# Performance work log

Measured on AMD Instinct MI355X. Metric: run time of the kernel, lower is better.

## Reference

```python
import jax, jax.numpy as jnp
import numpy as np
import math

B, S, D = 2, 4096, 1024
H, HD = 16, 64
R = 16

def _rope(x, cos, sin):
    # x: [B, S, H, HD]; cos/sin: [S, HD//2]
    xr = x.reshape(*x.shape[:-1], HD // 2, 2)
    xe, xo = xr[..., 0], xr[..., 1]
    c = cos[None, :, None, :]
    s = sin[None, :, None, :]
    # complex multiply (xe + i*xo) * (c + i*s)
    re = xe * c - xo * s
    im = xe * s + xo * c
    return jnp.stack([re, im], axis=-1).reshape(x.shape)

def setup_inputs() -> dict:
    key = jax.random.key(0)
    ks = jax.random.split(key, 20)
    inp = {}
    inp["x"] = jax.random.normal(ks[0], (B, S, D), dtype=jnp.float32)
    pos = jnp.arange(S, dtype=jnp.float32)
    inv_freq = 1.0 / (10000.0 ** (jnp.arange(0, HD, 2, dtype=jnp.float32) / HD))
    ang = pos[:, None] * inv_freq[None, :]  # [S, HD//2]
    inp["freqs_cos"] = jnp.cos(ang)
    inp["freqs_sin"] = jnp.sin(ang)
    causal = jnp.triu(jnp.full((S, S), -1e9, dtype=jnp.float32), k=1)
    inp["mask"] = causal[None, None, :, :]
    sc = 1.0 / math.sqrt(D)
    inp["wq_w"] = jax.random.normal(ks[1], (D, D), dtype=jnp.float32) * sc
    inp["wq_b"] = jnp.zeros((D,), dtype=jnp.float32)
    inp["wk_w"] = jax.random.normal(ks[2], (D, D), dtype=jnp.float32) * sc
    inp["wv_w"] = jax.random.normal(ks[3], (D, D), dtype=jnp.float32) * sc
    inp["wo_w"] = jax.random.normal(ks[4], (D, D), dtype=jnp.float32) * sc
    inp["wo_b"] = jnp.zeros((D,), dtype=jnp.float32)
    for i, nm in enumerate(["q", "k", "v", "o"]):
        inp[f"lora_{nm}_l1"] = jax.random.normal(ks[5 + 2 * i], (R, D), dtype=jnp.float32) * sc
        inp[f"lora_{nm}_l2"] = jax.random.normal(ks[6 + 2 * i], (D, R), dtype=jnp.float32) * 0.01
    return inp

def reference(x, freqs_cos, freqs_sin, mask, wq_w, wq_b, wk_w, wv_w, wo_w, wo_b,
              lora_q_l1, lora_q_l2, lora_k_l1, lora_k_l2,
              lora_v_l1, lora_v_l2, lora_o_l1, lora_o_l2):
    # QKV projections + LoRA deltas (torch Linear: y = x @ W.T + b, W is [out, in])
    xq = x @ wq_w.T + wq_b + (x @ lora_q_l1.T) @ lora_q_l2.T
    xk = x @ wk_w.T + (x @ lora_k_l1.T) @ lora_k_l2.T
    xv = x @ wv_w.T + (x @ lora_v_l1.T) @ lora_v_l2.T
    xq = xq.reshape(B, S, H, HD)
    xk = xk.reshape(B, S, H, HD)
    xv = xv.reshape(B, S, H, HD)
    xq = _rope(xq, freqs_cos, freqs_sin)
    xk = _rope(xk, freqs_cos, freqs_sin)
    # attention (training path: keys/values = current xk/xv, causal mask additive)
    scores = jnp.einsum('bqhd,bkhd->bhqk', xq, xk) / math.sqrt(HD)
    scores = scores + mask
    probs = jax.nn.softmax(scores.astype(jnp.float32), axis=-1).astype(xq.dtype)
    out = jnp.einsum('bhqk,bkhd->bqhd', probs, xv).reshape(B, S, D)
    return out @ wo_w.T + wo_b + (out @ lora_o_l1.T) @ lora_o_l2.T
```

## Files before the change

kernel.cpp:

```cpp
#include <hip/hip_runtime.h>
#include <hip/hip_bf16.h>
#include <stdint.h>

#define S_DIM 4096
#define D_DIM 1024
#define KAUG  1088
#define M_ROWS 8192

typedef short bf16x8 __attribute__((ext_vector_type(8)));
typedef float f32x4  __attribute__((ext_vector_type(4)));

__device__ __forceinline__ f32x4 mfma16(bf16x8 a, bf16x8 b, f32x4 c) {
  return __builtin_amdgcn_mfma_f32_16x16x32_bf16(a, b, c, 0, 0, 0);
}
__device__ __forceinline__ short f2bs(float f) {
  __hip_bfloat16 h = __float2bfloat16(f);
  return *reinterpret_cast<short*>(&h);
}
__device__ __forceinline__ short f2bs_fast(float f) {
  unsigned u = __builtin_bit_cast(unsigned, f) + 0x8000u;
  return (short)(u >> 16);
}
__device__ __forceinline__ unsigned pk2bf(float a, float b) {
  unsigned ua = __builtin_bit_cast(unsigned, a) + 0x8000u;
  unsigned ub = __builtin_bit_cast(unsigned, b) + 0x8000u;
  return __builtin_amdgcn_perm(ub, ua, 0x07060302);
}
__device__ __forceinline__ float bs2f(short s) {
  __hip_bfloat16 h;
  *reinterpret_cast<short*>(&h) = s;
  return __bfloat162float(h);
}
__device__ __forceinline__ float fexp2(float x) {
  return __builtin_amdgcn_exp2f(x);
}
__device__ __forceinline__ void gload16(const void* g, void* l) {
  __builtin_amdgcn_global_load_lds(
      (const __attribute__((address_space(1))) unsigned int*)g,
      (__attribute__((address_space(3))) unsigned int*)l, 16, 0, 0);
}

__global__ void prep_k(const float* __restrict__ x,
                       const float* __restrict__ wq, const float* __restrict__ wk,
                       const float* __restrict__ wv, const float* __restrict__ wo,
                       const float* __restrict__ wqb,
                       const float* __restrict__ lq1, const float* __restrict__ lq2,
                       const float* __restrict__ lk1, const float* __restrict__ lk2,
                       const float* __restrict__ lv1, const float* __restrict__ lv2,
                       const float* __restrict__ lo1, const float* __restrict__ lo2,
                       const float* __restrict__ cf, const float* __restrict__ sf,
                       short* __restrict__ xaug, short* __restrict__ wqkv,
                       short* __restrict__ woaug, short* __restrict__ l1cat,
                       float* __restrict__ biasc, float* __restrict__ cs2)
{
  unsigned i = blockIdx.x * 256u + threadIdx.x;
  if (i < 8388608u) {
    unsigned m = i >> 10, k = i & 1023u;
    xaug[(size_t)m * KAUG + k] = f2bs(x[i]);
    return;
  }
  i -= 8388608u;
  if (i < 3342336u) {
    unsigned n = i / 1088u, k = i - n * 1088u;
    float v;
    if (k < 1024u) {
      v = (n < 1024u) ? wq[n * 1024u + k]
        : (n < 2048u) ? wk[(n - 1024u) * 1024u + k]
                      : wv[(n - 2048u) * 1024u + k];
    } else {
      unsigned r = k - 1024u, blk = r >> 4, which = n >> 10;
      if (blk == which) {
        const float* l2 = which == 0 ? lq2 : which == 1 ? lk2 : lv2;
        v = l2[(n & 1023u) * 16u + (r & 15u)];
      } else v = 0.f;
    }
    wqkv[i] = f2bs(v);
    return;
  }
  i -= 3342336u;
  if (i < 1114112u) {
    unsigned n = i / 1088u, k = i - n * 1088u;
    float v = (k < 1024u) ? wo[n * 1024u + k]
            : (k < 1040u) ? lo2[n * 16u + (k - 1024u)] : 0.f;
    woaug[i] = f2bs(v);
    return;
  }
  i -= 1114112u;
  if (i < 65536u) {
    unsigned r = i >> 10, k = i & 1023u;
    const float* src = r < 16u ? lq1 : r < 32u ? lk1 : r < 48u ? lv1 : lo1;
    l1cat[i] = f2bs(src[(r & 15u) * 1024u + k]);
    return;
  }
  i -= 65536u;
  if (i < 3072u) {
    biasc[i] = (i < 1024u) ? wqb[i] : 0.f;
    return;
  }
  i -= 3072u;
  if (i < 131072u) {
    cs2[2u * i]     = cf[i];
    cs2[2u * i + 1] = sf[i];
  }
}

template<int MODE>
__global__ __launch_bounds__(256) void gemm_bt(
    const short* __restrict__ A, int lda,
    const short* __restrict__ B, int ldb,
    int N, int K,
    const float* __restrict__ bias,
    void* __restrict__ Cout, int ldc, int colofs,
    short* __restrict__ qo, short* __restrict__ ko, short* __restrict__ vo,
    const float* __restrict__ cs2)
{
  __shared__ short As[2][128 * 32];
  __shared__ short Bs[2][128 * 32];
  const int tid = threadIdx.x;
  const int w = tid >> 6, lane = tid & 63;
  const int q4 = lane >> 4, c = lane & 15;
  const int mh = w >> 1, nh = w & 1;

  const int id = (int)blockIdx.y * gridDim.x + (int)blockIdx.x;
  const int g = id & 7, j = id >> 3;
  const int mt = g * 8 + (j & 7);
  const int nt = j >> 3;

  const int rl = lane >> 2;
  const int kc = (lane & 3) * 8;

  const short* Ag0 = A + (size_t)(mt * 128 + w * 32 + rl) * lda + kc;
  const short* Ag1 = Ag0 + (size_t)16 * lda;
  int rb0 = nt * 128 + w * 32 + rl;      if (rb0 > N - 1) rb0 = N - 1;
  int rb1 = nt * 128 + w * 32 + 16 + rl; if (rb1 > N - 1) rb1 = N - 1;
  const short* Bg0 = B + (size_t)rb0 * ldb + kc;
  const short* Bg1 = B + (size_t)rb1 * ldb + kc;
  const int sD0 = (w * 32) * 32;
  const int sD1 = (w * 32 + 16) * 32;

  f32x4 acc[4][4];
#pragma unroll
  for (int ms = 0; ms < 4; ++ms)
#pragma unroll
    for (int ns = 0; ns < 4; ++ns) acc[ms][ns] = (f32x4){0.f, 0.f, 0.f, 0.f};

  gload16(Ag0, &As[0][sD0]);
  gload16(Ag1, &As[0][sD1]);
  gload16(Bg0, &Bs[0][sD0]);
  gload16(Bg1, &Bs[0][sD1]);
  Ag0 += 32; Ag1 += 32; Bg0 += 32; Bg1 += 32;
  __syncthreads();

  const int nkt = K >> 5;
  for (int kt = 0; kt < nkt; ++kt) {
    const int cur = kt & 1, nxt = cur ^ 1;
    if (kt + 1 < nkt) {
      gload16(Ag0, &As[nxt][sD0]);
      gload16(Ag1, &As[nxt][sD1]);
      gload16(Bg0, &Bs[nxt][sD0]);
      gload16(Bg1, &Bs[nxt][sD1]);
      Ag0 += 32; Ag1 += 32; Bg0 += 32; Bg1 += 32;
    }
    bf16x8 af[4], bfr[4];
#pragma unroll
    for (int ms = 0; ms < 4; ++ms)
      af[ms] = *(const bf16x8*)&As[cur][(mh * 64 + ms * 16 + c) * 32 + q4 * 8];
#pragma unroll
    for (int ns = 0; ns < 4; ++ns)
      bfr[ns] = *(const bf16x8*)&Bs[cur][(nh * 64 + ns * 16 + c) * 32 + q4 * 8];
#pragma unroll
    for (int ms = 0; ms < 4; ++ms)
#pragma unroll
      for (int ns = 0; ns < 4; ++ns)
        acc[ms][ns] = mfma16(af[ms], bfr[ns], acc[ms][ns]);
    __syncthreads();
  }

#pragma unroll
  for (int ms = 0; ms < 4; ++ms) {
#pragma unroll
    for (int ns = 0; ns < 4; ++ns) {
      const int n = nt * 128 + nh * 64 + ns * 16 + c;
      if (MODE == 0) {
        float bsv = (n < N) ? bias[n] : 0.f;
        float* Co = (float*)Cout;
#pragma unroll
        for (int r = 0; r < 4; ++r) {
          int m = mt * 128 + mh * 64 + ms * 16 + q4 * 4 + r;
          if (n < N) Co[(size_t)m * ldc + n] = acc[ms][ns][r] + bsv;
        }
      } else if (MODE == 1) {
        short* Co = (short*)Cout;
#pragma unroll
        for (int r = 0; r < 4; ++r) {
          int m = mt * 128 + mh * 64 + ms * 16 + q4 * 4 + r;
          if (n < N) Co[(size_t)m * ldc + colofs + n] = f2bs_fast(acc[ms][ns][r]);
        }
      } else {
        float bsv = bias[n];
        int which = n >> 10;
        int m0 = mt * 128 + mh * 64 + ms * 16 + q4 * 4;
        int bb = m0 >> 12, spos = m0 & 4095;
        if (which < 2) {
          int h = (n >> 6) & 15;
          int hd = n & 63;
          short* dst = which == 0 ? qo : ko;
          const float sgn = (c & 1) ? 1.f : -1.f;
          const int ihalf = hd >> 1;
#pragma unroll
          for (int r = 0; r < 4; ++r) {
            float val = acc[ms][ns][r] + bsv;
            float part = __shfl_xor(val, 1);
            float2 cs = *(const float2*)&cs2[((size_t)(spos + r) * 32 + ihalf) * 2];
            float res = val * cs.x + part * (sgn * cs.y);
            if (which == 0) res *= 0.18033688011112042f;
            dst[(size_t)((bb * 16 + h) * 4096 + spos + r) * 64 + hd] = f2bs_fast(res);
          }
        } else {
          int h = (n >> 6) & 15;
          int hd = n & 63;
          uint2 vk;
          vk.x = pk2bf(acc[ms][ns][0] + bsv, acc[ms][ns][1] + bsv);
          vk.y = pk2bf(acc[ms][ns][2] + bsv, acc[ms][ns][3] + bsv);
          *(uint2*)&vo[(((size_t)bb * 16 + h) * 64 + hd) * 4096 + spos] = vk;
        }
      }
    }
  }
}

template<int NT>
__global__ __launch_bounds__(256) void tgemm_k(
    const short* __restrict__ A, int lda,
    const short* __restrict__ B, int ldb,
    int N, int K, short* __restrict__ C, int ldc, int colofs)
{
  __shared__ short As[2][64 * 32];
  __shared__ short Bs[2][64 * 32];
  const int tid = threadIdx.x;
  const int w = tid >> 6, lane = tid & 63;
  const int q4 = lane >> 4, c = lane & 15;
  const int rl = lane >> 2, kc = (lane & 3) * 8;
  const int arow = w * 16 + rl;
  const int brow = arow <= N - 1 ? arow : N - 1;

  const short* Ag = A + (size_t)(blockIdx.x * 64 + arow) * lda + kc;
  const short* Bg = B + (size_t)brow * ldb + kc;
  const int sD = (w * 16) * 32;

  f32x4 acc[NT];
#pragma unroll
  for (int i = 0; i < NT; ++i) acc[i] = (f32x4){0.f, 0.f, 0.f, 0.f};

  gload16(Ag, &As[0][sD]);
  gload16(Bg, &Bs[0][sD]);
  Ag += 32; Bg += 32;
  __syncthreads();

  const int nkt = K >> 5;
  for (int kt = 0; kt < nkt; ++kt) {
    const int cur = kt & 1, nxt = cur ^ 1;
    if (kt + 1 < nkt) {
      gload16(Ag, &As[nxt][sD]);
      gload16(Bg, &Bs[nxt][sD]);
      Ag += 32; Bg += 32;
    }
    bf16x8 af = *(const bf16x8*)&As[cur][(w * 16 + c) * 32 + q4 * 8];
#pragma unroll
    for (int nsi = 0; nsi < NT; ++nsi) {
      bf16x8 bf = *(const bf16x8*)&Bs[cur][(nsi * 16 + c) * 32 + q4 * 8];
      acc[nsi] = mfma16(af, bf, acc[nsi]);
    }
    __syncthreads();
  }
#pragma unroll
  for (int nsi = 0; nsi < NT; ++nsi) {
#pragma unroll
    for (int r = 0; r < 4; ++r) {
      int m = blockIdx.x * 64 + w * 16 + q4 * 4 + r;
      int n = nsi * 16 + c;
      if (n < N) C[(size_t)m * ldc + colofs + n] = f2bs_fast(acc[nsi][r]);
    }
  }
}

__global__ __launch_bounds__(256, 2) void flash_k(
    const short* __restrict__ Qb, const short* __restrict__ Kb,
    const short* __restrict__ Vt, short* __restrict__ Oaug)
{
  __shared__ short lds[24576];
  short* const PL = &lds[16384];

  const int id = (int)blockIdx.y * 16 + (int)blockIdx.x;
  const int g = id & 7, j = id >> 3;
  const int bh = g * 4 + (j >> 4);
  const int bx = j & 15;

  const int tid = threadIdx.x;
  const int w = tid >> 6, lane = tid & 63;
  const int q4 = lane >> 4, c = lane & 15;

  const short* Kg = Kb + (size_t)bh * 4096 * 64;
  const short* Vg = Vt + (size_t)bh * 64 * 4096;

  const int l8 = lane >> 3, l7 = lane & 7;
  const int sw = (l7 ^ l8) * 8;
  const int G0 = w * 2, G1 = w * 2 + 1;
  const int koff0 = (G0 * 8 + l8) * 64 + sw;
  const int koff1 = (G1 * 8 + l8) * 64 + sw;
  const int voff0 = (G0 * 8 + l8) * 4096 + sw;
  const int voff1 = (G1 * 8 + l8) * 4096 + sw;
  const int qg = w * 4;
  const int qoff0 = ((qg + 0) * 8 + l8) * 64 + sw;
  const int qoff1 = ((qg + 1) * 8 + l8) * 64 + sw;
  const int qoff2 = ((qg + 2) * 8 + l8) * 64 + sw;
  const int qoff3 = ((qg + 3) * 8 + l8) * 64 + sw;

  const int c7 = c & 7;
  const int chA0 = ((q4) ^ c7) * 8;
  const int chA1 = ((4 + q4) ^ c7) * 8;
  const int rowc = c * 64;
  const int rowq = (w * 16 + c) * 64;
  const int pw_base = (w * 16 + c) * 64 + (q4 & 1) * 4;
  const int pw_g = q4 >> 1;

  const int b = bh >> 4, h = bh & 15;

  for (int half = 0; half < 2; ++half) {
    const int qt = half == 0 ? 31 - bx : bx;
    const short* Qg = Qb + ((size_t)bh * 4096 + qt * 128) * 64;

    gload16(Qg + qoff0, &lds[16384 + (qg + 0) * 512]);
    gload16(Qg + qoff1, &lds[16384 + (qg + 1) * 512]);
    gload16(Qg + qoff2, &lds[16384 + (qg + 2) * 512]);
    gload16(Qg + qoff3, &lds[16384 + (qg + 3) * 512]);
    gload16(Kg + koff0, &lds[G0 * 512]);
    gload16(Kg + koff1, &lds[G1 * 512]);
    gload16(Vg + voff0, &lds[8192 + G0 * 512]);
    gload16(Vg + voff1, &lds[8192 + G1 * 512]);
    __syncthreads();

    bf16x8 qa0 = *(const bf16x8*)(PL + rowq + chA0);
    bf16x8 qa1 = *(const bf16x8*)(PL + rowq + chA1);
    bf16x8 qb0 = *(const bf16x8*)(PL + 4096 + rowq + chA0);
    bf16x8 qb1 = *(const bf16x8*)(PL + 4096 + rowq + chA1);

    f32x4 oa[4], ob[4];
#pragma unroll
    for (int i = 0; i < 4; ++i) {
      oa[i] = (f32x4){0.f, 0.f, 0.f, 0.f};
      ob[i] = (f32x4){0.f, 0.f, 0.f, 0.f};
    }
    float la = 0.f, lb = 0.f;

    const int last = 2 * qt + 1;
    for (int kt = 0; kt <= last; ++kt) {
      const int cur = (kt & 1) * 4096;
      const short* Kc = &lds[cur];
      const short* Vc = &lds[8192 + cur];
      if (kt < last) {
        const int nxt = ((kt + 1) & 1) * 4096;
        const short* ks = Kg + (size_t)(kt + 1) * 4096;
        const short* vs = Vg + (size_t)(kt + 1) * 64;
        gload16(ks + koff0, &lds[nxt + G0 * 512]);
        gload16(ks + koff1, &lds[nxt + G1 * 512]);
        gload16(vs + voff0, &lds[8192 + nxt + G0 * 512]);
        gload16(vs + voff1, &lds[8192 + nxt + G1 * 512]);
      }
      const bool doA = (kt <= 2 * qt);

      f32x4 sa[4], sb[4];
#pragma unroll
      for (int ns = 0; ns < 4; ++ns) {
        bf16x8 kf0 = *(const bf16x8*)(Kc + ns * 1024 + rowc + chA0);
        bf16x8 kf1 = *(const bf16x8*)(Kc + ns * 1024 + rowc + chA1);
        sa[ns] = mfma16(kf0, qa0, (f32x4){0.f, 0.f, 0.f, 0.f});
        sa[ns] = mfma16(kf1, qa1, sa[ns]);
        sb[ns] = mfma16(kf0, qb0, (f32x4){0.f, 0.f, 0.f, 0.f});
        sb[ns] = mfma16(kf1, qb1, sb[ns]);
      }
      if (kt == 2 * qt) {
#pragma unroll
        for (int ns = 0; ns < 4; ++ns)
#pragma unroll
          for (int r = 0; r < 4; ++r)
            if (ns * 16 + q4 * 4 + r > w * 16 + c) sa[ns][r] = -1e30f;
      }
      if (kt == last) {
#pragma unroll
        for (int ns = 0; ns < 4; ++ns)
#pragma unroll
          for (int r = 0; r < 4; ++r)
            if (ns * 16 + q4 * 4 + r > w * 16 + c) sb[ns][r] = -1e30f;
      }

      bf16x8 pfa0, pfa1;
      if (doA) {
        float ps[4][4];
#pragma unroll
        for (int ns = 0; ns < 4; ++ns)
#pragma unroll
          for (int r = 0; r < 4; ++r) ps[ns][r] = fexp2(sa[ns][r]);
        float s0 = (ps[0][0] + ps[0][1]) + (ps[0][2] + ps[0][3]);
        float s1 = (ps[1][0] + ps[1][1]) + (ps[1][2] + ps[1][3]);
        float s2 = (ps[2][0] + ps[2][1]) + (ps[2][2] + ps[2][3]);
        float s3 = (ps[3][0] + ps[3][1]) + (ps[3][2] + ps[3][3]);
        float sum = (s0 + s1) + (s2 + s3);
        sum += __shfl_xor(sum, 16);
        sum += __shfl_xor(sum, 32);
        la += sum;
#pragma unroll
        for (int ns = 0; ns < 4; ++ns) {
          uint2 pk;
          pk.x = pk2bf(ps[ns][0], ps[ns][1]);
          pk.y = pk2bf(ps[ns][2], ps[ns][3]);
          *(uint2*)(PL + pw_base + (((ns * 2 + pw_g) ^ c7) * 8)) = pk;
        }
        pfa0 = *(const bf16x8*)(PL + rowq + chA0);
        pfa1 = *(const bf16x8*)(PL + rowq + chA1);
      }
      {
        float ps[4][4];
#pragma unroll
        for (int ns = 0; ns < 4; ++ns)
#pragma unroll
          for (int r = 0; r < 4; ++r) ps[ns][r] = fexp2(sb[ns][r]);
        float s0 = (ps[0][0] + ps[0][1]) + (ps[0][2] + ps[0][3]);
        float s1 = (ps[1][0] + ps[1][1]) + (ps[1][2] + ps[1][3]);
        float s2 = (ps[2][0] + ps[2][1]) + (ps[2][2] + ps[2][3]);
        float s3 = (ps[3][0] + ps[3][1]) + (ps[3][2] + ps[3][3]);
        float sum = (s0 + s1) + (s2 + s3);
        sum += __shfl_xor(sum, 16);
        sum += __shfl_xor(sum, 32);
        lb += sum;
#pragma unroll
        for (int ns = 0; ns < 4; ++ns) {
          uint2 pk;
          pk.x = pk2bf(ps[ns][0], ps[ns][1]);
          pk.y = pk2bf(ps[ns][2], ps[ns][3]);
          *(uint2*)(PL + 4096 + pw_base + (((ns * 2 + pw_g) ^ c7) * 8)) = pk;
        }
      }
      bf16x8 pfb0 = *(const bf16x8*)(PL + 4096 + rowq + chA0);
      bf16x8 pfb1 = *(const bf16x8*)(PL + 4096 + rowq + chA1);

#pragma unroll
      for (int nc = 0; nc < 4; ++nc) {
        bf16x8 vf0 = *(const bf16x8*)(Vc + nc * 1024 + rowc + chA0);
        bf16x8 vf1 = *(const bf16x8*)(Vc + nc * 1024 + rowc + chA1);
        if (doA) {
          oa[nc] = mfma16(vf0, pfa0, oa[nc]);
          oa[nc] = mfma16(vf1, pfa1, oa[nc]);
        }
        ob[nc] = mfma16(vf0, pfb0, ob[nc]);
        ob[nc] = mfma16(vf1, pfb1, ob[nc]);
      }
      __syncthreads();
    }

    float lia = 1.f / la, lib = 1.f / lb;
#pragma unroll
    for (int nc = 0; nc < 4; ++nc) {
      uint2 ok;
      ok.x = pk2bf(oa[nc][0] * lia, oa[nc][1] * lia);
      ok.y = pk2bf(oa[nc][2] * lia, oa[nc][3] * lia);
      *(uint2*)(PL + pw_base + (((nc * 2 + pw_g) ^ c7) * 8)) = ok;
      uint2 ok2;
      ok2.x = pk2bf(ob[nc][0] * lib, ob[nc][1] * lib);
      ok2.y = pk2bf(ob[nc][2] * lib, ob[nc][3] * lib);
      *(uint2*)(PL + 4096 + pw_base + (((nc * 2 + pw_g) ^ c7) * 8)) = ok2;
    }
    __syncthreads();
#pragma unroll
    for (int i2 = 0; i2 < 4; ++i2) {
      int ch = tid + i2 * 256;
      int r = ch >> 3, g2 = ch & 7;
      size_t row = (size_t)b * 4096 + qt * 128 + r;
      *(int4*)&Oaug[row * KAUG + h * 64 + g2 * 8] =
          *(const int4*)(PL + r * 64 + ((g2 ^ (r & 7)) * 8));
    }
    __syncthreads();
  }
}

extern "C" void kernel_launch(void* const* d_in, const int* in_sizes, int n_in,
                              void* d_out, int out_size, void* d_ws, size_t ws_size,
                              hipStream_t stream) {
  const float* x   = (const float*)d_in[0];
  const float* fc  = (const float*)d_in[1];
  const float* fs  = (const float*)d_in[2];
  const float* wq  = (const float*)d_in[4];
  const float* wqb = (const float*)d_in[5];
  const float* wk  = (const float*)d_in[6];
  const float* wv  = (const float*)d_in[7];
  const float* wo  = (const float*)d_in[8];
  const float* wob = (const float*)d_in[9];
  const float* lq1 = (const float*)d_in[10];
  const float* lq2 = (const float*)d_in[11];
  const float* lk1 = (const float*)d_in[12];
  const float* lk2 = (const float*)d_in[13];
  const float* lv1 = (const float*)d_in[14];
  const float* lv2 = (const float*)d_in[15];
  const float* lo1 = (const float*)d_in[16];
  const float* lo2 = (const float*)d_in[17];

  char* ws = (char*)d_ws;
  const size_t OFF_XAUG  = 0;
  const size_t OFF_XOAUG = 17825792;
  const size_t OFF_WQKV  = 35651584;
  const size_t OFF_WOAUG = 42336256;
  const size_t OFF_L1CAT = 44564480;
  const size_t OFF_BIASC = 44695552;
  const size_t OFF_QB    = 44707840;
  const size_t OFF_KB    = 61485056;
  const size_t OFF_VT    = 78262272;
  const size_t OFF_CS    = 95039488;

  short* xaug  = (short*)(ws + OFF_XAUG);
  short* xoaug = (short*)(ws + OFF_XOAUG);
  short* wqkv  = (short*)(ws + OFF_WQKV);
  short* woaug = (short*)(ws + OFF_WOAUG);
  short* l1cat = (short*)(ws + OFF_L1CAT);
  float* biasc = (float*)(ws + OFF_BIASC);
  short* qb    = (short*)(ws + OFF_QB);
  short* kb    = (short*)(ws + OFF_KB);
  short* vt    = (short*)(ws + OFF_VT);
  float* cs2   = (float*)(ws + OFF_CS);

  prep_k<<<50956, 256, 0, stream>>>(x, wq, wk, wv, wo, wqb,
                                    lq1, lq2, lk1, lk2, lv1, lv2, lo1, lo2,
                                    fc, fs,
                                    xaug, wqkv, woaug, l1cat, biasc, cs2);
  tgemm_k<3><<<128, 256, 0, stream>>>(xaug, KAUG, l1cat, 1024, 48, 1024,
                                      xaug, KAUG, 1024);
  gemm_bt<2><<<dim3(24, 64), 256, 0, stream>>>(xaug, KAUG, wqkv, KAUG, 3072, KAUG,
                                               biasc, nullptr, 0, 0, qb, kb, vt,
                                               cs2);
  flash_k<<<dim3(16, 32), 256, 0, stream>>>(qb, kb, vt, xoaug);
  tgemm_k<1><<<128, 256, 0, stream>>>(xoaug, KAUG, l1cat + 48 * 1024, 1024,
                                      16, 1024, xoaug, KAUG, 1024);
  gemm_bt<0><<<dim3(8, 64), 256, 0, stream>>>(xoaug, KAUG, woaug, KAUG, 1024, KAUG,
                                              wob, d_out, 1024, 0,
                                              nullptr, nullptr, nullptr, nullptr);
}
```

Before: 390.0 us.

## Fold LoRA deltas into effective weights instead of augmenting activations

The LoRA low-rank products are merged into the base weight matrices in the prep kernel (W + L2·L1), so the QKV and output GEMMs run with K=1024 instead of an augmented K=1088. This removes the two small tgemm launches that computed x·L1 and the extra 64 columns in each big GEMM, and shrinks the activation buffers. In exchange the prep kernel does 16 extra FMAs per weight element, and rounding the merged weights to bf16 changes numerics slightly.

```diff
diff --git a/kernel.cpp b/kernel.cpp
--- a/kernel.cpp
+++ b/kernel.cpp
@@ -4,7 +4,6 @@
 
 #define S_DIM 4096
 #define D_DIM 1024
-#define KAUG  1088
 #define M_ROWS 8192
 
 typedef short bf16x8 __attribute__((ext_vector_type(8)));
@@ -25,11 +24,6 @@
   unsigned ua = __builtin_bit_cast(unsigned, a) + 0x8000u;
   unsigned ub = __builtin_bit_cast(unsigned, b) + 0x8000u;
   return __builtin_amdgcn_perm(ub, ua, 0x07060302);
-}
-__device__ __forceinline__ float bs2f(short s) {
-  __hip_bfloat16 h;
-  *reinterpret_cast<short*>(&h) = s;
-  return __bfloat162float(h);
 }
 __device__ __forceinline__ float fexp2(float x) {
   return __builtin_amdgcn_exp2f(x);
@@ -50,49 +44,40 @@
                        const float* __restrict__ lo1, const float* __restrict__ lo2,
                        const float* __restrict__ cf, const float* __restrict__ sf,
                        short* __restrict__ xaug, short* __restrict__ wqkv,
-                       short* __restrict__ woaug, short* __restrict__ l1cat,
+                       short* __restrict__ woeff,
                        float* __restrict__ biasc, float* __restrict__ cs2)
 {
   unsigned i = blockIdx.x * 256u + threadIdx.x;
   if (i < 8388608u) {
-    unsigned m = i >> 10, k = i & 1023u;
-    xaug[(size_t)m * KAUG + k] = f2bs(x[i]);
+    xaug[i] = f2bs(x[i]);
     return;
   }
   i -= 8388608u;
-  if (i < 3342336u) {
-    unsigned n = i / 1088u, k = i - n * 1088u;
-    float v;
-    if (k < 1024u) {
-      v = (n < 1024u) ? wq[n * 1024u + k]
-        : (n < 2048u) ? wk[(n - 1024u) * 1024u + k]
-                      : wv[(n - 2048u) * 1024u + k];
-    } else {
-      unsigned r = k - 1024u, blk = r >> 4, which = n >> 10;
-      if (blk == which) {
-        const float* l2 = which == 0 ? lq2 : which == 1 ? lk2 : lv2;
-        v = l2[(n & 1023u) * 16u + (r & 15u)];
-      } else v = 0.f;
-    }
+  if (i < 3145728u) {
+    unsigned n = i >> 10, k = i & 1023u;
+    const float *wsrc, *l1, *l2;
+    unsigned nn;
+    if (n < 1024u)      { wsrc = wq; l1 = lq1; l2 = lq2; nn = n; }
+    else if (n < 2048u) { wsrc = wk; l1 = lk1; l2 = lk2; nn = n - 1024u; }
+    else                { wsrc = wv; l1 = lv1; l2 = lv2; nn = n - 2048u; }
+    float v = wsrc[nn * 1024u + k];
+#pragma unroll
+    for (unsigned r = 0; r < 16u; ++r)
+      v += l2[nn * 16u + r] * l1[r * 1024u + k];
     wqkv[i] = f2bs(v);
     return;
   }
-  i -= 3342336u;
-  if (i < 1114112u) {
-    unsigned n = i / 1088u, k = i - n * 1088u;
-    float v = (k < 1024u) ? wo[n * 1024u + k]
-            : (k < 1040u) ? lo2[n * 16u + (k - 1024u)] : 0.f;
-    woaug[i] = f2bs(v);
+  i -= 3145728u;
+  if (i < 1048576u) {
+    unsigned n = i >> 10, k = i & 1023u;
+    float v = wo[i];
+#pragma unroll
+    for (unsigned r = 0; r < 16u; ++r)
+      v += lo2[n * 16u + r] * lo1[r * 1024u + k];
+    woeff[i] = f2bs(v);
     return;
   }
-  i -= 1114112u;
-  if (i < 65536u) {
-    unsigned r = i >> 10, k = i & 1023u;
-    const float* src = r < 16u ? lq1 : r < 32u ? lk1 : r < 48u ? lv1 : lo1;
-    l1cat[i] = f2bs(src[(r & 15u) * 1024u + k]);
-    return;
-  }
-  i -= 65536u;
+  i -= 1048576u;
   if (i < 3072u) {
     biasc[i] = (i < 1024u) ? wqb[i] : 0.f;
     return;
@@ -229,61 +214,6 @@
   }
 }
 
-template<int NT>
-__global__ __launch_bounds__(256) void tgemm_k(
-    const short* __restrict__ A, int lda,
-    const short* __restrict__ B, int ldb,
-    int N, int K, short* __restrict__ C, int ldc, int colofs)
-{
-  __shared__ short As[2][64 * 32];
-  __shared__ short Bs[2][64 * 32];
-  const int tid = threadIdx.x;
-  const int w = tid >> 6, lane = tid & 63;
-  const int q4 = lane >> 4, c = lane & 15;
-  const int rl = lane >> 2, kc = (lane & 3) * 8;
-  const int arow = w * 16 + rl;
-  const int brow = arow <= N - 1 ? arow : N - 1;
-
-  const short* Ag = A + (size_t)(blockIdx.x * 64 + arow) * lda + kc;
-  const short* Bg = B + (size_t)brow * ldb + kc;
-  const int sD = (w * 16) * 32;
-
-  f32x4 acc[NT];
-#pragma unroll
-  for (int i = 0; i < NT; ++i) acc[i] = (f32x4){0.f, 0.f, 0.f, 0.f};
-
-  gload16(Ag, &As[0][sD]);
-  gload16(Bg, &Bs[0][sD]);
-  Ag += 32; Bg += 32;
-  __syncthreads();
-
-  const int nkt = K >> 5;
-  for (int kt = 0; kt < nkt; ++kt) {
-    const int cur = kt & 1, nxt = cur ^ 1;
-    if (kt + 1 < nkt) {
-      gload16(Ag, &As[nxt][sD]);
-      gload16(Bg, &Bs[nxt][sD]);
-      Ag += 32; Bg += 32;
-    }
-    bf16x8 af = *(const bf16x8*)&As[cur][(w * 16 + c) * 32 + q4 * 8];
-#pragma unroll
-    for (int nsi = 0; nsi < NT; ++nsi) {
-      bf16x8 bf = *(const bf16x8*)&Bs[cur][(nsi * 16 + c) * 32 + q4 * 8];
-      acc[nsi] = mfma16(af, bf, acc[nsi]);
-    }
-    __syncthreads();
-  }
-#pragma unroll
-  for (int nsi = 0; nsi < NT; ++nsi) {
-#pragma unroll
-    for (int r = 0; r < 4; ++r) {
-      int m = blockIdx.x * 64 + w * 16 + q4 * 4 + r;
-      int n = nsi * 16 + c;
-      if (n < N) C[(size_t)m * ldc + colofs + n] = f2bs_fast(acc[nsi][r]);
-    }
-  }
-}
-
 __global__ __launch_bounds__(256, 2) void flash_k(
     const short* __restrict__ Qb, const short* __restrict__ Kb,
     const short* __restrict__ Vt, short* __restrict__ Oaug)
@@ -476,7 +406,7 @@
       int ch = tid + i2 * 256;
       int r = ch >> 3, g2 = ch & 7;
       size_t row = (size_t)b * 4096 + qt * 128 + r;
-      *(int4*)&Oaug[row * KAUG + h * 64 + g2 * 8] =
+      *(int4*)&Oaug[row * 1024 + h * 64 + g2 * 8] =
           *(const int4*)(PL + r * 64 + ((g2 ^ (r & 7)) * 8));
     }
     __syncthreads();
@@ -506,40 +436,34 @@
 
   char* ws = (char*)d_ws;
   const size_t OFF_XAUG  = 0;
-  const size_t OFF_XOAUG = 17825792;
-  const size_t OFF_WQKV  = 35651584;
-  const size_t OFF_WOAUG = 42336256;
-  const size_t OFF_L1CAT = 44564480;
-  const size_t OFF_BIASC = 44695552;
-  const size_t OFF_QB    = 44707840;
-  const size_t OFF_KB    = 61485056;
-  const size_t OFF_VT    = 78262272;
-  const size_t OFF_CS    = 95039488;
+  const size_t OFF_XOAUG = 16777216;
+  const size_t OFF_WQKV  = 33554432;
+  const size_t OFF_WOEFF = 39845888;
+  const size_t OFF_BIASC = 41943040;
+  const size_t OFF_QB    = 41955328;
+  const size_t OFF_KB    = 58732544;
+  const size_t OFF_VT    = 75509760;
+  const size_t OFF_CS    = 92286976;
 
   short* xaug  = (short*)(ws + OFF_XAUG);
   short* xoaug = (short*)(ws + OFF_XOAUG);
   short* wqkv  = (short*)(ws + OFF_WQKV);
-  short* woaug = (short*)(ws + OFF_WOAUG);
-  short* l1cat = (short*)(ws + OFF_L1CAT);
+  short* woeff = (short*)(ws + OFF_WOEFF);
   float* biasc = (float*)(ws + OFF_BIASC);
   short* qb    = (short*)(ws + OFF_QB);
   short* kb    = (short*)(ws + OFF_KB);
   short* vt    = (short*)(ws + OFF_VT);
   float* cs2   = (float*)(ws + OFF_CS);
 
-  prep_k<<<50956, 256, 0, stream>>>(x, wq, wk, wv, wo, wqb,
+  prep_k<<<49676, 256, 0, stream>>>(x, wq, wk, wv, wo, wqb,
                                     lq1, lq2, lk1, lk2, lv1, lv2, lo1, lo2,
                                     fc, fs,
-                                    xaug, wqkv, woaug, l1cat, biasc, cs2);
-  tgemm_k<3><<<128, 256, 0, stream>>>(xaug, KAUG, l1cat, 1024, 48, 1024,
-                                      xaug, KAUG, 1024);
-  gemm_bt<2><<<dim3(24, 64), 256, 0, stream>>>(xaug, KAUG, wqkv, KAUG, 3072, KAUG,
+                                    xaug, wqkv, woeff, biasc, cs2);
+  gemm_bt<2><<<dim3(24, 64), 256, 0, stream>>>(xaug, 1024, wqkv, 1024, 3072, 1024,
                                                biasc, nullptr, 0, 0, qb, kb, vt,
                                                cs2);
   flash_k<<<dim3(16, 32), 256, 0, stream>>>(qb, kb, vt, xoaug);
-  tgemm_k<1><<<128, 256, 0, stream>>>(xoaug, KAUG, l1cat + 48 * 1024, 1024,
-                                      16, 1024, xoaug, KAUG, 1024);
-  gemm_bt<0><<<dim3(8, 64), 256, 0, stream>>>(xoaug, KAUG, woaug, KAUG, 1024, KAUG,
+  gemm_bt<0><<<dim3(8, 64), 256, 0, stream>>>(xoaug, 1024, woeff, 1024, 1024, 1024,
                                               wob, d_out, 1024, 0,
                                               nullptr, nullptr, nullptr, nullptr);
 }
```

Measured after the change: 365.4 us. 1.07x faster.
